# Kernel optimization log

Hardware: AMD Instinct MI355X
Metric: run time of the kernel (lower is better)

Reference implementation:

```python
import jax, jax.numpy as jnp
import numpy as np

H = 64  # hidden size hard-coded in the torch module


def _lstm_cell(x, h, c, Wih, Whh, b):
    # PyTorch LSTMCell: gates = x @ Wih.T + h @ Whh.T + bias_ih + bias_hh,
    # gate order (i, f, g, o), each of size H.
    gates = x @ Wih.T + h @ Whh.T + b
    i, f, g, o = jnp.split(gates, 4, axis=-1)
    c_new = jax.nn.sigmoid(f) * c + jax.nn.sigmoid(i) * jnp.tanh(g)
    h_new = jax.nn.sigmoid(o) * jnpp_tanh(c_new) if False else jax.nn.sigmoid(o) * jnp.tanh(c_new)
    return h_new, c_new


def setup_inputs() -> dict:
    key = jax.random.key(0)
    ks = jax.random.split(key, 12)
    B, T, F = 2048, 1024, 1
    s = 1.0 / np.sqrt(H)  # PyTorch LSTMCell/Linear init range

    def u(k, shape):
        return jax.random.uniform(k, shape, jnp.float32, -s, s)

    return {
        "input": jax.random.normal(ks[0], (B, T, F), jnp.float32),
        "Wih1": u(ks[1], (4 * H, F)),
        "Whh1": u(ks[2], (4 * H, H)),
        "bih1": u(ks[3], (4 * H,)),
        "bhh1": u(ks[4], (4 * H,)),
        "Wih2": u(ks[5], (4 * H, H)),
        "Whh2": u(ks[6], (4 * H, H)),
        "bih2": u(ks[7], (4 * H,)),
        "bhh2": u(ks[8], (4 * H,)),
        "Wl": u(ks[9], (1, H)),
        "bl": u(ks[10], (1,)),
        "future": 8,
    }


def reference(input, Wih1, Whh1, bih1, bhh1, Wih2, Whh2, bih2, bhh2, Wl, bl, future):
    B = input.shape[0]
    dtype = input.dtype
    z = jnp.zeros((B, H), dtype)
    b1 = bih1 + bhh1
    b2 = bih2 + bhh2

    def step(carry, x_t):
        h1, c1, h2, c2 = carry
        h1, c1 = _lstm_cell(x_t, h1, c1, Wih1, Whh1, b1)
        h2, c2 = _lstm_cell(h1, h2, c2, Wih2, Whh2, b2)
        return (h1, c1, h2, c2), None

    # scan over time: xs shaped [T, B, F]
    (h1, c1, h2, c2), _ = jax.lax.scan(step, (z, z, z, z), jnp.swapaxes(input, 0, 1))
    out = h2 @ Wl.T + bl  # readout from last input step

    def fstep(carry, _):
        out, h1, c1, h2, c2 = carry
        h1, c1 = _lstm_cell(out, h1, c1, Wih1, Whh1, b1)
        h2, c2 = _lstm_cell(h1, h2, c2, Wih2, Whh2, b2)
        out = h2 @ Wl.T + bl
        return (out, h1, c1, h2, c2), None

    (out, h1, c1, h2, c2), _ = jax.lax.scan(fstep, (out, h1, c1, h2, c2), None, length=future)
    return out[:, None, :]  # [B, 1, out_feature]
```

## Files before the change

### kernel.cpp

```cpp
#include <hip/hip_runtime.h>

#define HID 64
#define TSTEPS 1024
#define BPW 8
#define TW 512

typedef __attribute__((ext_vector_type(8))) short short8v;
typedef __attribute__((ext_vector_type(4))) float f32x4;

__device__ __forceinline__ unsigned short f2bf(float f) {
  unsigned u = __float_as_uint(f);
  u += 0x7FFFu + ((u >> 16) & 1u);
  return (unsigned short)(u >> 16);
}
__device__ __forceinline__ float bf2f(unsigned short h) {
  return __uint_as_float(((unsigned)h) << 16);
}
__device__ __forceinline__ float sigf(float x) {
  return __builtin_amdgcn_rcpf(1.0f + __expf(-x));
}
__device__ __forceinline__ float tanh_(float x) {
  return 1.0f - 2.0f * __builtin_amdgcn_rcpf(1.0f + __expf(2.0f * x));
}
__device__ __forceinline__ float dppror8(float x) {
  int xi = __float_as_int(x);
  int y = __builtin_amdgcn_update_dpp(xi, xi, 0x128, 0xF, 0xF, true);
  return __int_as_float(y);
}
__device__ __forceinline__ f32x4 mf(short8v a, short8v b, f32x4 c) {
  return __builtin_amdgcn_mfma_f32_16x16x32_bf16(a, b, c, 0, 0, 0);
}
__device__ __forceinline__ unsigned cvtpk_bf16(float a) {
  unsigned r;
  asm("v_cvt_pk_bf16_f32 %0, %1, %2" : "=v"(r) : "v"(a), "v"(a));
  return r;
}
__device__ __forceinline__ int frag_ld_off(int ss, int lane) {
  int byte = (ss * 64 + lane) * 16;
  byte ^= ((byte >> 7) & 7) << 4;
  return byte;
}
__device__ __forceinline__ int frag_addr16(int j, int col) {
  int byte = ((j >> 5) * 64 + ((j & 31) >> 3) * 16 + col) * 16 + (j & 7) * 2;
  byte ^= ((byte >> 7) & 7) << 4;
  return byte;
}
__device__ __forceinline__ void load8split(const float* rp, short8v& hi, short8v& lo) {
  float t[8];
#pragma unroll
  for (int e = 0; e < 8; ++e) t[e] = rp[e];
#pragma unroll
  for (int e = 0; e < 8; ++e) {
    unsigned short h = f2bf(t[e]);
    hi[e] = (short)h;
    lo[e] = (short)f2bf(t[e] - bf2f(h));
  }
}
__device__ __forceinline__ float cellup(float zi, float zf, float zg, float zo,
                                        float& c) {
  c = sigf(zf) * c + sigf(zi) * tanh_(zg);
  return sigf(zo) * tanh_(c);
}
__device__ __forceinline__ void fold2(const f32x4& a0, const f32x4& a1,
                                      bool dsel, float (&z)[4]) {
#pragma unroll
  for (int q = 0; q < 4; ++q) {
    float send = dsel ? a0[q] : a1[q];
    float own = dsel ? a1[q] : a0[q];
    z[q] = own + dppror8(send);
  }
}

struct __align__(128) SMem {
  float xin[TSTEPS + 1][BPW];
  short hf1[2][1024];
  short hf2[2][1024];
  float ro[8][BPW];
};

#define PIN6(a, b, c, d, e, f)                                              \
  asm volatile("" : "+v"(a), "+v"(b), "+v"(c), "+v"(d), "+v"(e), "+v"(f))

__global__ __launch_bounds__(TW, 2) void lstm2_kernel(
    const float* __restrict__ input, const float* __restrict__ Wih1,
    const float* __restrict__ Whh1, const float* __restrict__ bih1,
    const float* __restrict__ bhh1, const float* __restrict__ Wih2,
    const float* __restrict__ Whh2, const float* __restrict__ bih2,
    const float* __restrict__ bhh2, const float* __restrict__ Wl,
    const float* __restrict__ bl, const int* __restrict__ future,
    float* __restrict__ out) {
  __shared__ SMem s;
  const int tid = threadIdx.x;
  const int w = tid >> 6;
  const int lane = tid & 63;
  const int c = lane & 15;
  const int b = c & 7;
  const int d = (c >> 3) & 1;
  const int g = lane >> 4;
  const int jl = 4 * (2 * w + d) + g;
  const int b0 = blockIdx.x * BPW;

  short8v W1h[2][2], W1l[2][2];
  short8v W2h[2][2], W2l[2][2];
  short8v W3h[2][2], W3l[2][2];
#pragma unroll
  for (int tt = 0; tt < 2; ++tt) {
    const int T = 2 * w + tt;
    const int r16 = lane & 15;
    const int m = 64 * (r16 & 3) + 4 * T + (r16 >> 2);
    const int koff = (lane >> 4) * 8;
#pragma unroll
    for (int ss = 0; ss < 2; ++ss) {
      load8split(Whh1 + m * HID + ss * 32 + koff, W1h[tt][ss], W1l[tt][ss]);
      load8split(Wih2 + m * HID + ss * 32 + koff, W2h[tt][ss], W2l[tt][ss]);
      load8split(Whh2 + m * HID + ss * 32 + koff, W3h[tt][ss], W3l[tt][ss]);
    }
  }

  float bb1[4], wi1[4], bb2[4];
#pragma unroll
  for (int q = 0; q < 4; ++q) {
    const int row = 64 * q + jl;
    bb1[q] = bih1[row] + bhh1[row];
    wi1[q] = Wih1[row];
    bb2[q] = bih2[row] + bhh2[row];
  }
  const float wlv = Wl[jl];
  const float blv = bl[0];
  const int nfut = future[0];
  const int adr_hi = frag_addr16(jl, b);
  const int adr_lo = frag_addr16(jl, b + 8);
  const int off0 = frag_ld_off(0, lane);
  const int off1 = frag_ld_off(1, lane);

  {
    const float* src = input + (size_t)b0 * TSTEPS;
    for (int idx = tid; idx < BPW * TSTEPS; idx += TW) {
      int bi = idx >> 10;
      int t = idx & (TSTEPS - 1);
      s.xin[t][bi] = src[idx];
    }
    for (int idx = tid; idx < 2 * 1024; idx += TW) {
      ((short*)s.hf1)[idx] = 0;
      ((short*)s.hf2)[idx] = 0;
    }
  }
  const f32x4 zf = (f32x4){0.f, 0.f, 0.f, 0.f};
  f32x4 acc1_0 = zf, acc1_1 = zf;
  f32x4 acc2_0 = zf, acc2_1 = zf;
  float c1 = 0.f, c2 = 0.f;
  float h2n = 0.f;
  __syncthreads();

  const int total = TSTEPS + nfut;
  for (int sidx = 0; sidx < total; ++sidx) {
    const int p = sidx & 1, pn = p ^ 1;

    PIN6(W1h[0][0], W1h[0][1], W1h[1][0], W1h[1][1], W1l[0][0], W1l[0][1]);
    PIN6(W1l[1][0], W1l[1][1], W2h[0][0], W2h[0][1], W2h[1][0], W2h[1][1]);
    PIN6(W2l[0][0], W2l[0][1], W2l[1][0], W2l[1][1], W3h[0][0], W3h[0][1]);
    PIN6(W3h[1][0], W3h[1][1], W3l[0][0], W3l[0][1], W3l[1][0], W3l[1][1]);

    {
      const char* hb = (const char*)s.hf2[p];
      short8v B0 = *(const short8v*)(hb + off0);
      short8v B1 = *(const short8v*)(hb + off1);
      acc2_0 = mf(W3h[0][1], B1,
                  mf(W3l[0][1], B1, mf(W3h[0][0], B0, mf(W3l[0][0], B0, zf))));
      acc2_1 = mf(W3h[1][1], B1,
                  mf(W3l[1][1], B1, mf(W3h[1][0], B0, mf(W3l[1][0], B0, zf))));
    }
    {
      const int xt = (sidx < TSTEPS) ? sidx : TSTEPS;
      const float xv = s.xin[xt][b];
      float z[4];
      fold2(acc1_0, acc1_1, d, z);
#pragma unroll
      for (int q = 0; q < 4; ++q) z[q] += bb1[q] + xv * wi1[q];
      float h1n = cellup(z[0], z[1], z[2], z[3], c1);
      unsigned rh = cvtpk_bf16(h1n);
      float res = h1n - __uint_as_float(rh << 16);
      unsigned rl = cvtpk_bf16(res);
      char* hf1w = (char*)s.hf1[pn];
      *(short*)(hf1w + adr_hi) = (short)rh;
      *(short*)(hf1w + adr_lo) = (short)rl;
    }
    __syncthreads();

    {
      const char* cb = (const char*)s.hf1[pn];
      short8v C0 = *(const short8v*)(cb + off0);
      short8v C1 = *(const short8v*)(cb + off1);
      acc2_0 = mf(W2h[0][1], C1,
                  mf(W2l[0][1], C1, mf(W2h[0][0], C0, mf(W2l[0][0], C0, acc2_0))));
      acc2_1 = mf(W2h[1][1], C1,
                  mf(W2l[1][1], C1, mf(W2h[1][0], C0, mf(W2l[1][0], C0, acc2_1))));
      acc1_0 = mf(W1h[0][1], C1,
                  mf(W1l[0][1], C1, mf(W1h[0][0], C0, mf(W1l[0][0], C0, zf))));
      acc1_1 = mf(W1h[1][1], C1,
                  mf(W1l[1][1], C1, mf(W1h[1][0], C0, mf(W1l[1][0], C0, zf))));
      float z[4];
      fold2(acc2_0, acc2_1, d, z);
#pragma unroll
      for (int q = 0; q < 4; ++q) z[q] += bb2[q];
      h2n = cellup(z[0], z[1], z[2], z[3], c2);
      unsigned rh = cvtpk_bf16(h2n);
      float res = h2n - __uint_as_float(rh << 16);
      unsigned rl = cvtpk_bf16(res);
      char* hf2w = (char*)s.hf2[pn];
      *(short*)(hf2w + adr_hi) = (short)rh;
      *(short*)(hf2w + adr_lo) = (short)rl;
    }

    if (sidx >= TSTEPS - 1) {
      float v = wlv * h2n;
      v += __shfl_xor(v, 8, 64);
      v += __shfl_xor(v, 16, 64);
      v += __shfl_xor(v, 32, 64);
      if (lane < 8) s.ro[w][lane] = v;
      __syncthreads();
      if (tid < 8) {
        float t = blv;
#pragma unroll
        for (int k = 0; k < 8; ++k) t += s.ro[k][tid];
        s.xin[TSTEPS][tid] = t;
      }
    }
    __syncthreads();
  }

  if (tid < 8) out[b0 + tid] = s.xin[TSTEPS][tid];
}

extern "C" void kernel_launch(void* const* d_in, const int* in_sizes, int n_in,
                              void* d_out, int out_size, void* d_ws,
                              size_t ws_size, hipStream_t stream) {
  const float* input = (const float*)d_in[0];
  const float* Wih1 = (const float*)d_in[1];
  const float* Whh1 = (const float*)d_in[2];
  const float* bih1 = (const float*)d_in[3];
  const float* bhh1 = (const float*)d_in[4];
  const float* Wih2 = (const float*)d_in[5];
  const float* Whh2 = (const float*)d_in[6];
  const float* bih2 = (const float*)d_in[7];
  const float* bhh2 = (const float*)d_in[8];
  const float* Wl = (const float*)d_in[9];
  const float* bl = (const float*)d_in[10];
  const int* fut = (const int*)d_in[11];
  float* out = (float*)d_out;

  const int B = in_sizes[0] / TSTEPS;
  const int blocks = B / BPW;

  hipLaunchKernelGGL(lstm2_kernel, dim3(blocks), dim3(TW), 0, stream, input,
                     Wih1, Whh1, bih1, bhh1, Wih2, Whh2, bih2, bhh2, Wl, bl,
                     fut, out);
}
```

Measured before the change: 926.9 us.

## Halve workgroup to 4 waves, each wave handling two hidden-unit groups

The block shrinks from 8 to 4 waves. Each wave now owns two sets of hidden units (A and B), holding twice as many weight fragments in registers and issuing twice the MFMAs per step. The aim is to make each per-timestep __syncthreads barrier cheaper and to give each wave more independent MFMA work to hide latency. In exchange, register pressure doubles (48 short8v weight fragments), so launch bounds drop to 1 block per CU; spills or lower occupancy could offset the gain.

Result: slower. 1.044 ms (+12.7%).

```diff
diff --git a/kernel.cpp b/kernel.cpp
--- a/kernel.cpp
+++ b/kernel.cpp
@@ -3,7 +3,7 @@
 #define HID 64
 #define TSTEPS 1024
 #define BPW 8
-#define TW 512
+#define TW 256
 
 typedef __attribute__((ext_vector_type(8))) short short8v;
 typedef __attribute__((ext_vector_type(4))) float f32x4;
@@ -75,13 +75,12 @@
   float xin[TSTEPS + 1][BPW];
   short hf1[2][1024];
   short hf2[2][1024];
-  float ro[8][BPW];
+  float ro[4][BPW];
 };
 
-#define PIN6(a, b, c, d, e, f)                                              \
-  asm volatile("" : "+v"(a), "+v"(b), "+v"(c), "+v"(d), "+v"(e), "+v"(f))
-
-__global__ __launch_bounds__(TW, 2) void lstm2_kernel(
+#define PINV(v) asm volatile("" : "+v"(v))
+
+__global__ __launch_bounds__(TW, 1) void lstm2_kernel(
     const float* __restrict__ input, const float* __restrict__ Wih1,
     const float* __restrict__ Whh1, const float* __restrict__ bih1,
     const float* __restrict__ bhh1, const float* __restrict__ Wih2,
@@ -97,39 +96,56 @@
   const int b = c & 7;
   const int d = (c >> 3) & 1;
   const int g = lane >> 4;
-  const int jl = 4 * (2 * w + d) + g;
+  const int jlA = 4 * (4 * w + d) + g;
+  const int jlB = 4 * (4 * w + 2 + d) + g;
   const int b0 = blockIdx.x * BPW;
 
-  short8v W1h[2][2], W1l[2][2];
-  short8v W2h[2][2], W2l[2][2];
-  short8v W3h[2][2], W3l[2][2];
-#pragma unroll
-  for (int tt = 0; tt < 2; ++tt) {
-    const int T = 2 * w + tt;
-    const int r16 = lane & 15;
-    const int m = 64 * (r16 & 3) + 4 * T + (r16 >> 2);
-    const int koff = (lane >> 4) * 8;
-#pragma unroll
-    for (int ss = 0; ss < 2; ++ss) {
-      load8split(Whh1 + m * HID + ss * 32 + koff, W1h[tt][ss], W1l[tt][ss]);
-      load8split(Wih2 + m * HID + ss * 32 + koff, W2h[tt][ss], W2l[tt][ss]);
-      load8split(Whh2 + m * HID + ss * 32 + koff, W3h[tt][ss], W3l[tt][ss]);
-    }
-  }
-
-  float bb1[4], wi1[4], bb2[4];
+  short8v W1h[2][2][2], W1l[2][2][2];
+  short8v W2h[2][2][2], W2l[2][2][2];
+  short8v W3h[2][2][2], W3l[2][2][2];
+#pragma unroll
+  for (int P = 0; P < 2; ++P)
+#pragma unroll
+    for (int tt = 0; tt < 2; ++tt) {
+      const int T = 4 * w + 2 * P + tt;
+      const int r16 = lane & 15;
+      const int m = 64 * (r16 & 3) + 4 * T + (r16 >> 2);
+      const int koff = (lane >> 4) * 8;
+#pragma unroll
+      for (int ss = 0; ss < 2; ++ss) {
+        load8split(Whh1 + m * HID + ss * 32 + koff, W1h[P][tt][ss], W1l[P][tt][ss]);
+        load8split(Wih2 + m * HID + ss * 32 + koff, W2h[P][tt][ss], W2l[P][tt][ss]);
+        load8split(Whh2 + m * HID + ss * 32 + koff, W3h[P][tt][ss], W3l[P][tt][ss]);
+      }
+    }
+#pragma unroll
+  for (int P = 0; P < 2; ++P)
+#pragma unroll
+    for (int tt = 0; tt < 2; ++tt)
+#pragma unroll
+      for (int ss = 0; ss < 2; ++ss) {
+        PINV(W1h[P][tt][ss]); PINV(W1l[P][tt][ss]);
+        PINV(W2h[P][tt][ss]); PINV(W2l[P][tt][ss]);
+        PINV(W3h[P][tt][ss]); PINV(W3l[P][tt][ss]);
+      }
+
+  float bb1A[4], wi1A[4], bb2A[4], bb1B[4], wi1B[4], bb2B[4];
 #pragma unroll
   for (int q = 0; q < 4; ++q) {
-    const int row = 64 * q + jl;
-    bb1[q] = bih1[row] + bhh1[row];
-    wi1[q] = Wih1[row];
-    bb2[q] = bih2[row] + bhh2[row];
-  }
-  const float wlv = Wl[jl];
+    const int rA = 64 * q + jlA;
+    const int rB = 64 * q + jlB;
+    bb1A[q] = bih1[rA] + bhh1[rA];
+    wi1A[q] = Wih1[rA];
+    bb2A[q] = bih2[rA] + bhh2[rA];
+    bb1B[q] = bih1[rB] + bhh1[rB];
+    wi1B[q] = Wih1[rB];
+    bb2B[q] = bih2[rB] + bhh2[rB];
+  }
+  const float wlA = Wl[jlA], wlB = Wl[jlB];
   const float blv = bl[0];
   const int nfut = future[0];
-  const int adr_hi = frag_addr16(jl, b);
-  const int adr_lo = frag_addr16(jl, b + 8);
+  const int adrA_hi = frag_addr16(jlA, b), adrA_lo = frag_addr16(jlA, b + 8);
+  const int adrB_hi = frag_addr16(jlB, b), adrB_lo = frag_addr16(jlB, b + 8);
   const int off0 = frag_ld_off(0, lane);
   const int off1 = frag_ld_off(1, lane);
 
@@ -146,44 +162,54 @@
     }
   }
   const f32x4 zf = (f32x4){0.f, 0.f, 0.f, 0.f};
-  f32x4 acc1_0 = zf, acc1_1 = zf;
-  f32x4 acc2_0 = zf, acc2_1 = zf;
-  float c1 = 0.f, c2 = 0.f;
-  float h2n = 0.f;
+  f32x4 acc1[2][2], acc2[2][2];
+#pragma unroll
+  for (int P = 0; P < 2; ++P)
+#pragma unroll
+    for (int tt = 0; tt < 2; ++tt) {
+      acc1[P][tt] = zf;
+      acc2[P][tt] = zf;
+    }
+  float c1A = 0.f, c1B = 0.f, c2A = 0.f, c2B = 0.f;
+  float h2nA = 0.f, h2nB = 0.f;
   __syncthreads();
 
   const int total = TSTEPS + nfut;
   for (int sidx = 0; sidx < total; ++sidx) {
     const int p = sidx & 1, pn = p ^ 1;
-
-    PIN6(W1h[0][0], W1h[0][1], W1h[1][0], W1h[1][1], W1l[0][0], W1l[0][1]);
-    PIN6(W1l[1][0], W1l[1][1], W2h[0][0], W2h[0][1], W2h[1][0], W2h[1][1]);
-    PIN6(W2l[0][0], W2l[0][1], W2l[1][0], W2l[1][1], W3h[0][0], W3h[0][1]);
-    PIN6(W3h[1][0], W3h[1][1], W3l[0][0], W3l[0][1], W3l[1][0], W3l[1][1]);
 
     {
       const char* hb = (const char*)s.hf2[p];
       short8v B0 = *(const short8v*)(hb + off0);
       short8v B1 = *(const short8v*)(hb + off1);
-      acc2_0 = mf(W3h[0][1], B1,
-                  mf(W3l[0][1], B1, mf(W3h[0][0], B0, mf(W3l[0][0], B0, zf))));
-      acc2_1 = mf(W3h[1][1], B1,
-                  mf(W3l[1][1], B1, mf(W3h[1][0], B0, mf(W3l[1][0], B0, zf))));
-    }
-    {
+#pragma unroll
+      for (int P = 0; P < 2; ++P)
+#pragma unroll
+        for (int tt = 0; tt < 2; ++tt)
+          acc2[P][tt] = mf(W3h[P][tt][1], B1,
+                           mf(W3l[P][tt][1], B1,
+                              mf(W3h[P][tt][0], B0, mf(W3l[P][tt][0], B0, zf))));
       const int xt = (sidx < TSTEPS) ? sidx : TSTEPS;
       const float xv = s.xin[xt][b];
-      float z[4];
-      fold2(acc1_0, acc1_1, d, z);
-#pragma unroll
-      for (int q = 0; q < 4; ++q) z[q] += bb1[q] + xv * wi1[q];
-      float h1n = cellup(z[0], z[1], z[2], z[3], c1);
-      unsigned rh = cvtpk_bf16(h1n);
-      float res = h1n - __uint_as_float(rh << 16);
-      unsigned rl = cvtpk_bf16(res);
+      float zA[4], zB[4];
+      fold2(acc1[0][0], acc1[0][1], d, zA);
+      fold2(acc1[1][0], acc1[1][1], d, zB);
+#pragma unroll
+      for (int q = 0; q < 4; ++q) {
+        zA[q] += bb1A[q] + xv * wi1A[q];
+        zB[q] += bb1B[q] + xv * wi1B[q];
+      }
+      float h1nA = cellup(zA[0], zA[1], zA[2], zA[3], c1A);
+      float h1nB = cellup(zB[0], zB[1], zB[2], zB[3], c1B);
+      unsigned rhA = cvtpk_bf16(h1nA);
+      unsigned rlA = cvtpk_bf16(h1nA - __uint_as_float(rhA << 16));
+      unsigned rhB = cvtpk_bf16(h1nB);
+      unsigned rlB = cvtpk_bf16(h1nB - __uint_as_float(rhB << 16));
       char* hf1w = (char*)s.hf1[pn];
-      *(short*)(hf1w + adr_hi) = (short)rh;
-      *(short*)(hf1w + adr_lo) = (short)rl;
+      *(short*)(hf1w + adrA_hi) = (short)rhA;
+      *(short*)(hf1w + adrA_lo) = (short)rlA;
+      *(short*)(hf1w + adrB_hi) = (short)rhB;
+      *(short*)(hf1w + adrB_lo) = (short)rlB;
     }
     __syncthreads();
 
@@ -191,29 +217,44 @@
       const char* cb = (const char*)s.hf1[pn];
       short8v C0 = *(const short8v*)(cb + off0);
       short8v C1 = *(const short8v*)(cb + off1);
-      acc2_0 = mf(W2h[0][1], C1,
-                  mf(W2l[0][1], C1, mf(W2h[0][0], C0, mf(W2l[0][0], C0, acc2_0))));
-      acc2_1 = mf(W2h[1][1], C1,
-                  mf(W2l[1][1], C1, mf(W2h[1][0], C0, mf(W2l[1][0], C0, acc2_1))));
-      acc1_0 = mf(W1h[0][1], C1,
-                  mf(W1l[0][1], C1, mf(W1h[0][0], C0, mf(W1l[0][0], C0, zf))));
-      acc1_1 = mf(W1h[1][1], C1,
-                  mf(W1l[1][1], C1, mf(W1h[1][0], C0, mf(W1l[1][0], C0, zf))));
-      float z[4];
-      fold2(acc2_0, acc2_1, d, z);
-#pragma unroll
-      for (int q = 0; q < 4; ++q) z[q] += bb2[q];
-      h2n = cellup(z[0], z[1], z[2], z[3], c2);
-      unsigned rh = cvtpk_bf16(h2n);
-      float res = h2n - __uint_as_float(rh << 16);
-      unsigned rl = cvtpk_bf16(res);
+#pragma unroll
+      for (int P = 0; P < 2; ++P)
+#pragma unroll
+        for (int tt = 0; tt < 2; ++tt)
+          acc2[P][tt] = mf(W2h[P][tt][1], C1,
+                           mf(W2l[P][tt][1], C1,
+                              mf(W2h[P][tt][0], C0,
+                                 mf(W2l[P][tt][0], C0, acc2[P][tt]))));
+#pragma unroll
+      for (int P = 0; P < 2; ++P)
+#pragma unroll
+        for (int tt = 0; tt < 2; ++tt)
+          acc1[P][tt] = mf(W1h[P][tt][1], C1,
+                           mf(W1l[P][tt][1], C1,
+                              mf(W1h[P][tt][0], C0, mf(W1l[P][tt][0], C0, zf))));
+      float zA[4], zB[4];
+      fold2(acc2[0][0], acc2[0][1], d, zA);
+      fold2(acc2[1][0], acc2[1][1], d, zB);
+#pragma unroll
+      for (int q = 0; q < 4; ++q) {
+        zA[q] += bb2A[q];
+        zB[q] += bb2B[q];
+      }
+      h2nA = cellup(zA[0], zA[1], zA[2], zA[3], c2A);
+      h2nB = cellup(zB[0], zB[1], zB[2], zB[3], c2B);
+      unsigned rhA = cvtpk_bf16(h2nA);
+      unsigned rlA = cvtpk_bf16(h2nA - __uint_as_float(rhA << 16));
+      unsigned rhB = cvtpk_bf16(h2nB);
+      unsigned rlB = cvtpk_bf16(h2nB - __uint_as_float(rhB << 16));
       char* hf2w = (char*)s.hf2[pn];
-      *(short*)(hf2w + adr_hi) = (short)rh;
-      *(short*)(hf2w + adr_lo) = (short)rl;
+      *(short*)(hf2w + adrA_hi) = (short)rhA;
+      *(short*)(hf2w + adrA_lo) = (short)rlA;
+      *(short*)(hf2w + adrB_hi) = (short)rhB;
+      *(short*)(hf2w + adrB_lo) = (short)rlB;
     }
 
     if (sidx >= TSTEPS - 1) {
-      float v = wlv * h2n;
+      float v = wlA * h2nA + wlB * h2nB;
       v += __shfl_xor(v, 8, 64);
       v += __shfl_xor(v, 16, 64);
       v += __shfl_xor(v, 32, 64);
@@ -222,7 +263,7 @@
       if (tid < 8) {
         float t = blv;
 #pragma unroll
-        for (int k = 0; k < 8; ++k) t += s.ro[k][tid];
+        for (int k = 0; k < 4; ++k) t += s.ro[k][tid];
         s.xin[TSTEPS][tid] = t;
       }
     }
```
